# Optimization experiments

Measured on AMD Instinct MI355X. Metric: run time of the kernel, lower is better.

The kernel has to match this reference:

```python
import jax, jax.numpy as jnp
import numpy as np

TEMPERATURE = 0.5
EPS = 1e-8  # torch F.cosine_similarity norm clamp
B, D = 4096, 768


def setup_inputs() -> dict:
    key = jax.random.key(0)
    k1, k2 = jax.random.split(key)
    return {
        "aug_hidden1": jax.random.normal(k1, (B, D), dtype=jnp.float32),
        "aug_hidden2": jax.random.normal(k2, (B, D), dtype=jnp.float32),
    }


def reference(aug_hidden1, aug_hidden2):
    b = aug_hidden1.shape[0]
    n = 2 * b
    h = jnp.concatenate([aug_hidden1, aug_hidden2], axis=0)  # [N, D]
    norm = jnp.maximum(jnp.linalg.norm(h, axis=1, keepdims=True), EPS)
    hn = h / norm
    # cosine-similarity matrix via GEMM (equivalent to broadcasted cosine_similarity)
    sim = jnp.matmul(hn, hn.T) / TEMPERATURE  # [N, N]
    idx = jnp.arange(n)
    pos = sim[idx, (idx + b) % n]  # positives: sim(i, i+B) and sim(i+B, i)
    # row logits = {positive} U {all entries except diagonal and pair} = all off-diagonal
    # entries, so CrossEntropy(label=0) == logsumexp(off-diagonal row) - positive
    sim_masked = jnp.where(jnp.eye(n, dtype=bool), -jnp.inf, sim)
    lse = jax.nn.logsumexp(sim_masked, axis=1)  # [N]
    return jnp.mean(lse - pos)
```

## Files before the change

### kernel.cpp

```cpp
#include <hip/hip_runtime.h>
#include <hip/hip_bf16.h>


#define B_SZ 4096
#define D_SZ 768
#define N_SZ 8192
#define ROWB 384
constexpr float INV_T = 2.0f;

typedef float f32x16 __attribute__((ext_vector_type(16)));
typedef int i32x8 __attribute__((ext_vector_type(8)));
typedef int i32x4 __attribute__((ext_vector_type(4)));
typedef __attribute__((address_space(1))) const unsigned int gu32;
typedef __attribute__((address_space(3))) unsigned int lu32;

__device__ inline void async16(const void* g, void* l) {
    __builtin_amdgcn_global_load_lds((gu32*)g, (lu32*)l, 16, 0, 0);
}

__device__ inline float hsum32_dpp(float x) {
    float s = x, t;
    t = __int_as_float(__builtin_amdgcn_update_dpp(0, __float_as_int(s), 0x111, 0xf, 0xf, true)); s += t;
    t = __int_as_float(__builtin_amdgcn_update_dpp(0, __float_as_int(s), 0x112, 0xf, 0xf, true)); s += t;
    t = __int_as_float(__builtin_amdgcn_update_dpp(0, __float_as_int(s), 0x114, 0xf, 0xf, true)); s += t;
    t = __int_as_float(__builtin_amdgcn_update_dpp(0, __float_as_int(s), 0x118, 0xf, 0xf, true)); s += t;
    t = __int_as_float(__builtin_amdgcn_update_dpp(0, __float_as_int(s), 0x142, 0xa, 0xf, true)); s += t;
    return s;
}

__device__ inline unsigned fp4_enc(float v) {
    float a = fabsf(v);
    unsigned c;
    if (a < 1.25f)      c = (a < 0.25f) ? 0u : (a < 0.75f) ? 1u : 2u;
    else if (a < 2.5f)  c = (a < 1.75f) ? 3u : 4u;
    else                c = (a < 3.5f) ? 5u : (a < 5.0f) ? 6u : 7u;
    return c | (v < 0.f ? 8u : 0u);
}

__global__ __launch_bounds__(256) void prep_k(const float* __restrict__ h1,
                                              const float* __restrict__ h2,
                                              unsigned char* __restrict__ hn4,
                                              float* __restrict__ pos,
                                              float* __restrict__ out) {
    if (blockIdx.x == 0 && threadIdx.x == 0) out[0] = 0.f;
    const int i = blockIdx.x * 4 + (threadIdx.x >> 6);
    const int lane = threadIdx.x & 63;
    const float4* a4 = (const float4*)(h1 + (size_t)i * D_SZ);
    const float4* b4 = (const float4*)(h2 + (size_t)i * D_SZ);
    float4 av[3], bv[3];
    float sa = 0.f, sb = 0.f, dt = 0.f;
#pragma unroll
    for (int j = 0; j < 3; ++j) {
        av[j] = a4[lane * 3 + j];
        bv[j] = b4[lane * 3 + j];
        sa += av[j].x * av[j].x + av[j].y * av[j].y + av[j].z * av[j].z + av[j].w * av[j].w;
        sb += bv[j].x * bv[j].x + bv[j].y * bv[j].y + bv[j].z * bv[j].z + bv[j].w * bv[j].w;
        dt += av[j].x * bv[j].x + av[j].y * bv[j].y + av[j].z * bv[j].z + av[j].w * bv[j].w;
    }
#pragma unroll
    for (int m = 1; m < 64; m <<= 1) {
        sa += __shfl_xor(sa, m, 64);
        sb += __shfl_xor(sb, m, 64);
        dt += __shfl_xor(dt, m, 64);
    }
    const float n1 = fmaxf(sqrtf(sa), 1e-8f), n2 = fmaxf(sqrtf(sb), 1e-8f);
    const float i1 = 1.0f / n1, i2 = 1.0f / n2;
    const float s1 = i1 * 16.0f, s2 = i2 * 16.0f;
    unsigned short* d1 = (unsigned short*)(hn4 + (size_t)i * ROWB);
    unsigned short* d2 = (unsigned short*)(hn4 + (size_t)(i + B_SZ) * ROWB);
#pragma unroll
    for (int j = 0; j < 3; ++j) {
        float va[4] = {av[j].x, av[j].y, av[j].z, av[j].w};
        float vb[4] = {bv[j].x, bv[j].y, bv[j].z, bv[j].w};
        unsigned u1 = 0, u2 = 0;
#pragma unroll
        for (int e = 0; e < 4; ++e) {
            u1 |= fp4_enc(va[e] * s1) << (4 * e);
            u2 |= fp4_enc(vb[e] * s2) << (4 * e);
        }
        d1[lane * 3 + j] = (unsigned short)u1;
        d2[lane * 3 + j] = (unsigned short)u2;
    }
    if (lane == 0) {
        float p = dt * i1 * i2 * INV_T;
        pos[i] = p;
        pos[i + B_SZ] = p;
    }
}

#define BM 128
#define SLAB 4096
#define SPW 3
#define WINB 96
#define NWIN 4
#define BUFS 12288

__global__ __launch_bounds__(512) void gemm_reduce_k(const unsigned char* __restrict__ hn4,
                                                     float* __restrict__ part) {
    __shared__ __align__(16) unsigned char As[2 * BUFS];
    __shared__ __align__(16) unsigned char Bs[2 * BUFS];
    const int b0 = blockIdx.x;
    const int b = (b0 & 7) * 260 + (b0 >> 3);
    int tx = (int)((sqrtf(8.0f * (float)b + 1.0f) - 1.0f) * 0.5f);
    while ((tx + 1) * (tx + 2) / 2 <= b) ++tx;
    while (tx * (tx + 1) / 2 > b) --tx;
    const int ty = b - tx * (tx + 1) / 2;
    const int rowBase = ty * BM;
    const int colBase = tx * BM;
    const bool diagBlk = (ty == tx);

    const int tid = threadIdx.x;
    const int wave = tid >> 6;
    const int lane = tid & 63;
    const int l32 = lane & 31;
    const int half = lane >> 5;
    const int ms = wave & 3;
    const int nh = wave >> 2;

    f32x16 acc[2];
#pragma unroll
    for (int nt = 0; nt < 2; ++nt)
#pragma unroll
        for (int j = 0; j < 16; ++j) acc[nt][j] = 0.f;

    const bool stB = wave >= 4;
    const int cg = (lane & 1) ^ ((lane >> 3) & 1);
    const unsigned char* gsrc =
        hn4 + (size_t)((stB ? colBase : rowBase) + ms * 32 + (lane >> 1)) * ROWB + cg * 16;
    unsigned char* ldst = (stB ? Bs : As) + ms * 1024;

    const int p = half ^ ((l32 >> 2) & 1);
    const int aOff = (ms * 32 + l32) * 32 + p * 16;
    const int bOff = (nh * 64 + l32) * 32 + p * 16;

#pragma unroll
    for (int s = 0; s < SPW; ++s)
        async16(gsrc + s * 32, ldst + s * SLAB);
    __syncthreads();

    for (int w = 0; w < NWIN; ++w) {
        const int buf = w & 1;
        if (w + 1 < NWIN) {
            const unsigned char* g0 = gsrc + (w + 1) * WINB;
            unsigned char* l0 = ldst + (buf ^ 1) * BUFS;
#pragma unroll
            for (int s = 0; s < SPW; ++s)
                async16(g0 + s * 32, l0 + s * SLAB);
        }
        const unsigned char* Ab = As + buf * BUFS;
        const unsigned char* Bb = Bs + buf * BUFS;
#pragma unroll
        for (int s = 0; s < SPW; ++s) {
            i32x4 al = *(const i32x4*)(Ab + s * SLAB + aOff);
            i32x8 a = {al[0], al[1], al[2], al[3], 0, 0, 0, 0};
#pragma unroll
            for (int nt = 0; nt < 2; ++nt) {
                i32x4 bl = *(const i32x4*)(Bb + s * SLAB + bOff + nt * 1024);
                i32x8 bf = {bl[0], bl[1], bl[2], bl[3], 0, 0, 0, 0};
                acc[nt] = __builtin_amdgcn_mfma_scale_f32_32x32x64_f8f6f4(
                    a, bf, acc[nt], 4, 4, 0, 0x7C7C7C7C, 0, 0x7B7B7B7B);
            }
        }
        __syncthreads();
    }

    float* rowS = (float*)As;
    float* colS = (float*)(As + 1024);
    float rs[16];
#pragma unroll
    for (int j = 0; j < 16; ++j) rs[j] = 0.f;
    float csum[2] = {0.f, 0.f};
#pragma unroll
    for (int nt = 0; nt < 2; ++nt) {
        const int col = colBase + nh * 64 + nt * 32 + l32;
#pragma unroll
        for (int j = 0; j < 16; ++j) {
            const int row = rowBase + ms * 32 + (j & 3) + 8 * (j >> 2) + 4 * half;
            float e = __expf(acc[nt][j]);
            e = (diagBlk && row == col) ? 0.f : e;
            rs[j] += e;
            csum[nt] += e;
        }
    }
#pragma unroll
    for (int j = 0; j < 16; ++j) rs[j] = hsum32_dpp(rs[j]);
    if (l32 == 31) {
#pragma unroll
        for (int j = 0; j < 16; ++j)
            rowS[nh * 128 + ms * 32 + (j & 3) + 8 * (j >> 2) + 4 * half] = rs[j];
    }
#pragma unroll
    for (int nt = 0; nt < 2; ++nt) {
        float c = csum[nt] + __shfl_xor(csum[nt], 32, 64);
        if (half == 0) colS[ms * 128 + nh * 64 + nt * 32 + l32] = c;
    }
    __syncthreads();
    if (tid < 128) {
        part[((size_t)ty * 64 + tx) * 128 + tid] = rowS[tid] + rowS[128 + tid];
    } else if (tid < 256 && !diagBlk) {
        const int c = tid - 128;
        part[((size_t)tx * 64 + ty) * 128 + c] =
            colS[c] + colS[128 + c] + colS[256 + c] + colS[384 + c];
    }
}

__global__ __launch_bounds__(128) void finalize_k(const float* __restrict__ part,
                                                  const float* __restrict__ pos,
                                                  float* __restrict__ out) {
    __shared__ float red[2];
    const int t = blockIdx.x;
    const int r = threadIdx.x;
    const float* p = part + (size_t)t * 64 * 128 + r;
    float s = 0.f;
#pragma unroll 16
    for (int u = 0; u < 64; ++u) s += p[u * 128];
    const int i = t * 128 + r;
    float v = __logf(s) - pos[i];
#pragma unroll
    for (int m = 1; m < 64; m <<= 1) v += __shfl_xor(v, m, 64);
    if ((r & 63) == 0) red[r >> 6] = v;
    __syncthreads();
    if (r == 0) atomicAdd(out, (red[0] + red[1]) * (1.0f / (float)N_SZ));
}

extern "C" void kernel_launch(void* const* d_in, const int* in_sizes, int n_in,
                              void* d_out, int out_size, void* d_ws, size_t ws_size,
                              hipStream_t stream) {
    const float* h1 = (const float*)d_in[0];
    const float* h2 = (const float*)d_in[1];
    float* out = (float*)d_out;

    char* ws = (char*)d_ws;
    unsigned char* hn4 = (unsigned char*)ws;
    float* pos  = (float*)(ws + (size_t)N_SZ * ROWB);
    float* part = (float*)(ws + (size_t)N_SZ * ROWB + 32768);

    prep_k<<<B_SZ / 4, 256, 0, stream>>>(h1, h2, hn4, pos, out);
    const int nTiles = N_SZ / BM;
    const int nBlocks = nTiles * (nTiles + 1) / 2;
    gemm_reduce_k<<<nBlocks, 512, 0, stream>>>(hn4, part);
    finalize_k<<<64, 128, 0, stream>>>(part, pos, out);
}
```

Baseline: 100.6 us.

## Use 256x128 tiles over the symmetric sim matrix with staircase diagonal masking

Changes the GEMM tile from 128x128 to 256x128 (8 waves each owning 32 rows and 4 column subtiles), and enumerates the upper-triangular region in 256-row strips with a new block mapping. Tiles that straddle the diagonal mask the lower triangle, and the partial-sum layout and finalize loops are rewritten to match. The goal is more MFMA work per LDS byte and fewer blocks, at the cost of extra accumulator registers and some redundant compute in the straddling tiles.

```diff
diff --git a/kernel.cpp b/kernel.cpp
--- a/kernel.cpp
+++ b/kernel.cpp
@@ -88,74 +88,83 @@
     }
 }
 
-#define BM 128
-#define SLAB 4096
-#define SPW 3
-#define WINB 96
-#define NWIN 4
-#define BUFS 12288
+#define WINB 64
+#define NWIN 6
+#define ASLB 8192
+#define BSLB 4096
+#define ABUF 16384
+#define BBUF 8192
 
 __global__ __launch_bounds__(512) void gemm_reduce_k(const unsigned char* __restrict__ hn4,
                                                      float* __restrict__ part) {
-    __shared__ __align__(16) unsigned char As[2 * BUFS];
-    __shared__ __align__(16) unsigned char Bs[2 * BUFS];
+    __shared__ __align__(16) unsigned char As[2 * ABUF];
+    __shared__ __align__(16) unsigned char Bs[2 * BBUF];
     const int b0 = blockIdx.x;
-    const int b = (b0 & 7) * 260 + (b0 >> 3);
-    int tx = (int)((sqrtf(8.0f * (float)b + 1.0f) - 1.0f) * 0.5f);
-    while ((tx + 1) * (tx + 2) / 2 <= b) ++tx;
-    while (tx * (tx + 1) / 2 > b) --tx;
-    const int ty = b - tx * (tx + 1) / 2;
-    const int rowBase = ty * BM;
-    const int colBase = tx * BM;
-    const bool diagBlk = (ty == tx);
+    const int b = (b0 & 7) * 132 + (b0 >> 3);
+    int I = (int)((65.0f - sqrtf(65.0f * 65.0f - 4.0f * (float)b)) * 0.5f);
+    while (65 * (I + 1) - (I + 1) * (I + 1) <= b) ++I;
+    while (65 * I - I * I > b) --I;
+    const int J = 2 * I + (b - (65 * I - I * I));
+    const int rowBase = I * 256;
+    const int colBase = J * 128;
+    const bool strad = ((J >> 1) == I);
 
     const int tid = threadIdx.x;
     const int wave = tid >> 6;
     const int lane = tid & 63;
     const int l32 = lane & 31;
     const int half = lane >> 5;
-    const int ms = wave & 3;
-    const int nh = wave >> 2;
-
-    f32x16 acc[2];
-#pragma unroll
-    for (int nt = 0; nt < 2; ++nt)
+
+    f32x16 acc[4];
+#pragma unroll
+    for (int nt = 0; nt < 4; ++nt)
 #pragma unroll
         for (int j = 0; j < 16; ++j) acc[nt][j] = 0.f;
 
-    const bool stB = wave >= 4;
     const int cg = (lane & 1) ^ ((lane >> 3) & 1);
-    const unsigned char* gsrc =
-        hn4 + (size_t)((stB ? colBase : rowBase) + ms * 32 + (lane >> 1)) * ROWB + cg * 16;
-    unsigned char* ldst = (stB ? Bs : As) + ms * 1024;
+    const unsigned char* gU[3];
+    unsigned char* lU[3];
+    int strU[3];
+#pragma unroll
+    for (int k = 0; k < 3; ++k) {
+        const int u = wave * 3 + k;
+        if (u < 16) {
+            const int sa = u >> 3, rg = u & 7;
+            gU[k] = hn4 + (size_t)(rowBase + rg * 32 + (lane >> 1)) * ROWB + sa * 32 + cg * 16;
+            lU[k] = As + sa * ASLB + rg * 1024;
+            strU[k] = ABUF;
+        } else {
+            const int v = u - 16, sb = v >> 2, rg = v & 3;
+            gU[k] = hn4 + (size_t)(colBase + rg * 32 + (lane >> 1)) * ROWB + sb * 32 + cg * 16;
+            lU[k] = Bs + sb * BSLB + rg * 1024;
+            strU[k] = BBUF;
+        }
+    }
 
     const int p = half ^ ((l32 >> 2) & 1);
-    const int aOff = (ms * 32 + l32) * 32 + p * 16;
-    const int bOff = (nh * 64 + l32) * 32 + p * 16;
-
-#pragma unroll
-    for (int s = 0; s < SPW; ++s)
-        async16(gsrc + s * 32, ldst + s * SLAB);
+    const int aOff = (wave * 32 + l32) * 32 + p * 16;
+    const int bOff = l32 * 32 + p * 16;
+
+#pragma unroll
+    for (int k = 0; k < 3; ++k) async16(gU[k], lU[k]);
     __syncthreads();
 
     for (int w = 0; w < NWIN; ++w) {
         const int buf = w & 1;
         if (w + 1 < NWIN) {
-            const unsigned char* g0 = gsrc + (w + 1) * WINB;
-            unsigned char* l0 = ldst + (buf ^ 1) * BUFS;
-#pragma unroll
-            for (int s = 0; s < SPW; ++s)
-                async16(g0 + s * 32, l0 + s * SLAB);
-        }
-        const unsigned char* Ab = As + buf * BUFS;
-        const unsigned char* Bb = Bs + buf * BUFS;
-#pragma unroll
-        for (int s = 0; s < SPW; ++s) {
-            i32x4 al = *(const i32x4*)(Ab + s * SLAB + aOff);
+#pragma unroll
+            for (int k = 0; k < 3; ++k)
+                async16(gU[k] + (w + 1) * WINB, lU[k] + (buf ^ 1) * strU[k]);
+        }
+        const unsigned char* Ab = As + buf * ABUF;
+        const unsigned char* Bb = Bs + buf * BBUF;
+#pragma unroll
+        for (int s = 0; s < 2; ++s) {
+            i32x4 al = *(const i32x4*)(Ab + s * ASLB + aOff);
             i32x8 a = {al[0], al[1], al[2], al[3], 0, 0, 0, 0};
 #pragma unroll
-            for (int nt = 0; nt < 2; ++nt) {
-                i32x4 bl = *(const i32x4*)(Bb + s * SLAB + bOff + nt * 1024);
+            for (int nt = 0; nt < 4; ++nt) {
+                i32x4 bl = *(const i32x4*)(Bb + s * BSLB + bOff + nt * 1024);
                 i32x8 bf = {bl[0], bl[1], bl[2], bl[3], 0, 0, 0, 0};
                 acc[nt] = __builtin_amdgcn_mfma_scale_f32_32x32x64_f8f6f4(
                     a, bf, acc[nt], 4, 4, 0, 0x7C7C7C7C, 0, 0x7B7B7B7B);
@@ -169,15 +178,15 @@
     float rs[16];
 #pragma unroll
     for (int j = 0; j < 16; ++j) rs[j] = 0.f;
-    float csum[2] = {0.f, 0.f};
-#pragma unroll
-    for (int nt = 0; nt < 2; ++nt) {
-        const int col = colBase + nh * 64 + nt * 32 + l32;
+    float csum[4] = {0.f, 0.f, 0.f, 0.f};
+#pragma unroll
+    for (int nt = 0; nt < 4; ++nt) {
+        const int col = colBase + nt * 32 + l32;
 #pragma unroll
         for (int j = 0; j < 16; ++j) {
-            const int row = rowBase + ms * 32 + (j & 3) + 8 * (j >> 2) + 4 * half;
+            const int row = rowBase + wave * 32 + (j & 3) + 8 * (j >> 2) + 4 * half;
             float e = __expf(acc[nt][j]);
-            e = (diagBlk && row == col) ? 0.f : e;
+            e = (strad && row >= col) ? 0.f : e;
             rs[j] += e;
             csum[nt] += e;
         }
@@ -187,20 +196,23 @@
     if (l32 == 31) {
 #pragma unroll
         for (int j = 0; j < 16; ++j)
-            rowS[nh * 128 + ms * 32 + (j & 3) + 8 * (j >> 2) + 4 * half] = rs[j];
-    }
-#pragma unroll
-    for (int nt = 0; nt < 2; ++nt) {
+            rowS[wave * 32 + (j & 3) + 8 * (j >> 2) + 4 * half] = rs[j];
+    }
+#pragma unroll
+    for (int nt = 0; nt < 4; ++nt) {
         float c = csum[nt] + __shfl_xor(csum[nt], 32, 64);
-        if (half == 0) colS[ms * 128 + nh * 64 + nt * 32 + l32] = c;
+        if (half == 0) colS[wave * 128 + nt * 32 + l32] = c;
     }
     __syncthreads();
-    if (tid < 128) {
-        part[((size_t)ty * 64 + tx) * 128 + tid] = rowS[tid] + rowS[128 + tid];
-    } else if (tid < 256 && !diagBlk) {
-        const int c = tid - 128;
-        part[((size_t)tx * 64 + ty) * 128 + c] =
-            colS[c] + colS[128 + c] + colS[256 + c] + colS[384 + c];
+    if (tid < 256) {
+        const int a = 2 * I + (tid >> 7);
+        part[((size_t)a * 96 + J) * 128 + (tid & 127)] = rowS[tid];
+    } else if (tid < 384) {
+        const int c = tid - 256;
+        float v = 0.f;
+#pragma unroll
+        for (int wv = 0; wv < 8; ++wv) v += colS[wv * 128 + c];
+        part[((size_t)J * 96 + 64 + I) * 128 + c] = v;
     }
 }
 
@@ -208,13 +220,14 @@
                                                   const float* __restrict__ pos,
                                                   float* __restrict__ out) {
     __shared__ float red[2];
-    const int t = blockIdx.x;
+    const int a = blockIdx.x;
     const int r = threadIdx.x;
-    const float* p = part + (size_t)t * 64 * 128 + r;
+    const int h = a >> 1;
+    const float* p = part + (size_t)a * 96 * 128 + r;
     float s = 0.f;
-#pragma unroll 16
-    for (int u = 0; u < 64; ++u) s += p[u * 128];
-    const int i = t * 128 + r;
+    for (int j = 2 * h; j < 64; ++j) s += p[(size_t)j * 128];
+    for (int i2 = 0; i2 <= h; ++i2) s += p[(size_t)(64 + i2) * 128];
+    const int i = a * 128 + r;
     float v = __logf(s) - pos[i];
 #pragma unroll
     for (int m = 1; m < 64; m <<= 1) v += __shfl_xor(v, m, 64);
@@ -236,8 +249,6 @@
     float* part = (float*)(ws + (size_t)N_SZ * ROWB + 32768);
 
     prep_k<<<B_SZ / 4, 256, 0, stream>>>(h1, h2, hn4, pos, out);
-    const int nTiles = N_SZ / BM;
-    const int nBlocks = nTiles * (nTiles + 1) / 2;
-    gemm_reduce_k<<<nBlocks, 512, 0, stream>>>(hn4, part);
+    gemm_reduce_k<<<1056, 512, 0, stream>>>(hn4, part);
     finalize_k<<<64, 128, 0, stream>>>(part, pos, out);
 }
```

Measured after the change: 131.9 us. +31.2%, slower.
